# Optimization experiments

Measured on AMD Instinct MI355X. Metric: run time of the kernel, lower is better.

Reference implementation:

```python
import jax, jax.numpy as jnp
import numpy as np

IN_DIM = 512
C_OUT = IN_DIM // 8  # 64
B, H, W = 8, 128, 128


def setup_inputs() -> dict:
    key = jax.random.key(0)
    ks = jax.random.split(key, 6)
    x = jax.random.normal(ks[0], (B, IN_DIM, H, W), dtype=jnp.float32)
    # 1x1 conv weights stored as [out_ch, in_ch] matrices (kernel size 1)
    qkv_w = jax.random.normal(ks[1], (3 * C_OUT, IN_DIM), dtype=jnp.float32) * (1.0 / np.sqrt(IN_DIM))
    qkv_b = jax.random.normal(ks[2], (3 * C_OUT,), dtype=jnp.float32) * 0.01
    out_w = jax.random.normal(ks[3], (IN_DIM, C_OUT), dtype=jnp.float32) * (1.0 / np.sqrt(C_OUT))
    out_b = jax.random.normal(ks[4], (IN_DIM,), dtype=jnp.float32) * 0.01
    # gamma is init to 0 in torch; use a small nonzero value so both paths are exercised
    gamma = jnp.asarray(0.5, dtype=jnp.float32)
    return {"x": x, "qkv_w": qkv_w, "qkv_b": qkv_b, "out_w": out_w, "out_b": out_b, "gamma": gamma}


def reference(x, qkv_w, qkv_b, out_w, out_b, gamma):
    # qkv_conv: 1x1 conv == channel matmul
    qkv = jnp.einsum('bchw,oc->bohw', x, qkv_w) + qkv_b[None, :, None, None]
    q, k, v = jnp.split(qkv, 3, axis=1)  # each [B, C', H, W]

    # Horizontal branch: per column w, channel-channel attention contracting over H
    energy_h = jnp.einsum('bqhw,bkhw->bwqk', q, k)          # [B, W, C', C']
    attn_h = jax.nn.softmax(energy_h, axis=-1)
    out_h = jnp.einsum('bwqk,bkhw->bqhw', attn_h, v)        # [B, C', H, W]

    # Vertical branch: per row h, channel-channel attention contracting over W
    energy_v = jnp.einsum('bqhw,bkhw->bhqk', q, k)          # [B, H, C', C']
    attn_v = jax.nn.softmax(energy_v, axis=-1)
    out_v = jnp.einsum('bhqk,bkhw->bqhw', attn_v, v)        # [B, C', H, W]

    out = gamma * (out_h + out_v)
    out = jnp.einsum('bchw,oc->bohw', out, out_w) + out_b[None, :, None, None]
    return out + x
```

## Files before the change

kernel.cpp:

```cpp
#include <hip/hip_runtime.h>


typedef _Float16 f16;
typedef _Float16 f16x8 __attribute__((ext_vector_type(8)));
typedef float f32x4 __attribute__((ext_vector_type(4)));

#define MFMA16(a, b, c) __builtin_amdgcn_mfma_f32_16x16x32_f16(a, b, c, 0, 0, 0)

constexpr int CIN = 512;
constexpr int COUT = 64;
constexpr int HW = 128;
constexpr int P = HW * HW;
constexpr int QKV_CH = 192;

__global__ __launch_bounds__(256) void qkv_gemm(
    const float* __restrict__ x, const float* __restrict__ w,
    const float* __restrict__ bias, f16* __restrict__ qkv)
{
  __shared__ __attribute__((aligned(16))) f16 Wl[64 * 40];
  __shared__ __attribute__((aligned(16))) f16 Xt[128 * 40];
  const int m0 = blockIdx.x * 64;
  const int p0 = blockIdx.y * 128;
  const int b = blockIdx.z;
  const float* xb = x + (size_t)b * CIN * P;
  const int t = threadIdx.x;
  const int lane = t & 63, wv = t >> 6;
  const int quad = lane >> 4, l15 = lane & 15;
  const int wm = (wv >> 1) * 32, wn = (wv & 1) * 64;

  f32x4 acc[2][4] = {};
  for (int k0 = 0; k0 < CIN; k0 += 32) {
    for (int it = 0; it < 2; ++it) {
      int c = t + it * 256;
      int row = c >> 3, c4 = (c & 7) * 4;
      const float4 v = *(const float4*)(w + (size_t)(m0 + row) * CIN + k0 + c4);
      f16* d = &Wl[row * 40 + c4];
      d[0] = (f16)v.x; d[1] = (f16)v.y; d[2] = (f16)v.z; d[3] = (f16)v.w;
    }
    for (int it = 0; it < 4; ++it) {
      int c = t + it * 256;
      int kr = c >> 5, p4 = (c & 31) * 4;
      const float4 v = *(const float4*)(xb + (size_t)(k0 + kr) * P + p0 + p4);
      float vv[4] = {v.x, v.y, v.z, v.w};
#pragma unroll
      for (int j = 0; j < 4; ++j) {
        int p = p4 + j;
        int kc = kr ^ (((p >> 3) & 3) << 3);
        Xt[p * 40 + kc] = (f16)vv[j];
      }
    }
    __syncthreads();
    f16x8 af[2], bf[4];
#pragma unroll
    for (int ms = 0; ms < 2; ++ms)
      af[ms] = *(const f16x8*)&Wl[(wm + ms * 16 + l15) * 40 + quad * 8];
#pragma unroll
    for (int ns = 0; ns < 4; ++ns) {
      int pr = wn + ns * 16 + l15;
      int kb = (quad * 8) ^ (((pr >> 3) & 3) << 3);
      bf[ns] = *(const f16x8*)&Xt[pr * 40 + kb];
    }
#pragma unroll
    for (int ms = 0; ms < 2; ++ms)
#pragma unroll
      for (int ns = 0; ns < 4; ++ns)
        acc[ms][ns] = MFMA16(af[ms], bf[ns], acc[ms][ns]);
    __syncthreads();
  }
  f16* ob = qkv + (size_t)b * QKV_CH * P;
#pragma unroll
  for (int ms = 0; ms < 2; ++ms) {
    int mbase = m0 + wm + ms * 16 + quad * 4;
#pragma unroll
    for (int r = 0; r < 4; ++r) {
      float bi = bias[mbase + r];
#pragma unroll
      for (int ns = 0; ns < 4; ++ns) {
        int p = p0 + wn + ns * 16 + l15;
        ob[(size_t)(mbase + r) * P + p] = (f16)(acc[ms][ns][r] + bi);
      }
    }
  }
}

__global__ __launch_bounds__(256) void transpose_hw(
    const f16* __restrict__ in, f16* __restrict__ out)
{
  __shared__ __attribute__((aligned(16))) f16 T[64 * 72];
  const size_t plane = blockIdx.x;
  const int r0 = blockIdx.y * 64, c0 = blockIdx.z * 64;
  const f16* ip = in + plane * P;
  f16* op = out + plane * P;
  const int t = threadIdx.x;
  for (int it = 0; it < 2; ++it) {
    int c = t + it * 256;
    int row = c >> 3, c8 = (c & 7) * 8;
    *(f16x8*)&T[row * 72 + c8] =
        *(const f16x8*)(ip + (size_t)(r0 + row) * HW + c0 + c8);
  }
  __syncthreads();
  for (int it = 0; it < 2; ++it) {
    int c = t + it * 256;
    int wr = c >> 3, h8 = (c & 7) * 8;
    f16 tmp[8];
#pragma unroll
    for (int j = 0; j < 8; ++j) tmp[j] = T[(h8 + j) * 72 + wr];
    *(f16x8*)(op + (size_t)(c0 + wr) * HW + r0 + h8) = *(const f16x8*)tmp;
  }
}

__global__ __launch_bounds__(256) void cc_attn(
    const f16* __restrict__ qkvT, const f16* __restrict__ qkvN,
    f16* __restrict__ outT, f16* __restrict__ outN)
{
  __shared__ __attribute__((aligned(16))) f16 smem[64 * 136 * 2 + 128 * 72];
  f16* Ql = smem;
  f16* Kl = smem + 64 * 136;
  f16* Vt = smem + 2 * 64 * 136;
  f16* Al = smem;
  const int s = blockIdx.x, b = blockIdx.y;
  const f16* src = blockIdx.z ? qkvN : qkvT;
  f16* dst = blockIdx.z ? outN : outT;
  const f16* base = src + (size_t)b * QKV_CH * P + (size_t)s * HW;
  const int t = threadIdx.x;
  const int lane = t & 63, wv = t >> 6;
  const int quad = lane >> 4, l15 = lane & 15;

  for (int it = 0; it < 4; ++it) {
    int c = t + it * 256;
    int row = c >> 4, c8 = (c & 15) * 8;
    *(f16x8*)&Ql[row * 136 + c8] = *(const f16x8*)(base + (size_t)row * P + c8);
    *(f16x8*)&Kl[row * 136 + c8] =
        *(const f16x8*)(base + (size_t)(64 + row) * P + c8);
    f16x8 v = *(const f16x8*)(base + (size_t)(128 + row) * P + c8);
#pragma unroll
    for (int j = 0; j < 8; ++j) {
      int h = c8 + j;
      int kc = row ^ (((h >> 3) & 7) << 3);
      Vt[h * 72 + kc] = v[j];
    }
  }
  __syncthreads();

  const int m0 = wv * 16;
  f32x4 e[4] = {};
#pragma unroll
  for (int kk = 0; kk < 4; ++kk) {
    f16x8 aq = *(const f16x8*)&Ql[(m0 + l15) * 136 + kk * 32 + quad * 8];
#pragma unroll
    for (int nt = 0; nt < 4; ++nt) {
      f16x8 bk = *(const f16x8*)&Kl[(nt * 16 + l15) * 136 + kk * 32 + quad * 8];
      e[nt] = MFMA16(aq, bk, e[nt]);
    }
  }
  float pr[4][4];
  float rinv[4];
#pragma unroll
  for (int r = 0; r < 4; ++r) {
    float mx = fmaxf(fmaxf(e[0][r], e[1][r]), fmaxf(e[2][r], e[3][r]));
    for (int off = 1; off < 16; off <<= 1) mx = fmaxf(mx, __shfl_xor(mx, off));
    float sm = 0.f;
#pragma unroll
    for (int nt = 0; nt < 4; ++nt) {
      float pv = __expf(e[nt][r] - mx);
      pr[nt][r] = pv;
      sm += pv;
    }
    for (int off = 1; off < 16; off <<= 1) sm += __shfl_xor(sm, off);
    rinv[r] = 1.0f / sm;
  }
  __syncthreads();
#pragma unroll
  for (int nt = 0; nt < 4; ++nt)
#pragma unroll
    for (int r = 0; r < 4; ++r)
      Al[(m0 + quad * 4 + r) * 72 + nt * 16 + l15] = (f16)(pr[nt][r] * rinv[r]);
  __syncthreads();

  f32x4 o[8] = {};
#pragma unroll
  for (int kk = 0; kk < 2; ++kk) {
    f16x8 ap = *(const f16x8*)&Al[(m0 + l15) * 72 + kk * 32 + quad * 8];
#pragma unroll
    for (int nt = 0; nt < 8; ++nt) {
      int hr = nt * 16 + l15;
      int kb = (kk * 32 + quad * 8) ^ (((hr >> 3) & 7) << 3);
      f16x8 bv = *(const f16x8*)&Vt[hr * 72 + kb];
      o[nt] = MFMA16(ap, bv, o[nt]);
    }
  }
  f16* db = dst + (size_t)b * COUT * P + (size_t)s * HW;
#pragma unroll
  for (int nt = 0; nt < 8; ++nt)
#pragma unroll
    for (int r = 0; r < 4; ++r)
      db[(size_t)(m0 + quad * 4 + r) * P + nt * 16 + l15] = (f16)o[nt][r];
}

__global__ __launch_bounds__(256) void out_proj(
    const f16* __restrict__ ah, const f16* __restrict__ av,
    const float* __restrict__ w, const float* __restrict__ bias,
    const float* __restrict__ gamma_p, const float* __restrict__ x,
    float* __restrict__ out)
{
  __shared__ __attribute__((aligned(16))) f16 Wl[64 * 72];
  __shared__ __attribute__((aligned(16))) f16 St[128 * 72];
  const int m0 = blockIdx.x * 64;
  const int p0 = blockIdx.y * 128;
  const int b = blockIdx.z;
  const int t = threadIdx.x;
  const int lane = t & 63, wv = t >> 6;
  const int quad = lane >> 4, l15 = lane & 15;
  const int wm = (wv >> 1) * 32, wn = (wv & 1) * 64;

  for (int it = 0; it < 4; ++it) {
    int c = t + it * 256;
    int row = c >> 4, c4 = (c & 15) * 4;
    const float4 v = *(const float4*)(w + (size_t)(m0 + row) * COUT + c4);
    f16* d = &Wl[row * 72 + c4];
    d[0] = (f16)v.x; d[1] = (f16)v.y; d[2] = (f16)v.z; d[3] = (f16)v.w;
  }
  const size_t abase = (size_t)b * COUT * P + p0;
  for (int it = 0; it < 4; ++it) {
    int c = t + it * 256;
    int k = c >> 4, p8 = (c & 15) * 8;
    f16x8 a = *(const f16x8*)(ah + abase + (size_t)k * P + p8);
    f16x8 vv = *(const f16x8*)(av + abase + (size_t)k * P + p8);
#pragma unroll
    for (int j = 0; j < 8; ++j) {
      int p = p8 + j;
      int kc = k ^ (((p >> 3) & 7) << 3);
      St[p * 72 + kc] = (f16)(a[j] + vv[j]);
    }
  }
  __syncthreads();

  f32x4 acc[2][4] = {};
#pragma unroll
  for (int kk = 0; kk < 2; ++kk) {
    f16x8 af[2], bf[4];
#pragma unroll
    for (int ms = 0; ms < 2; ++ms)
      af[ms] = *(const f16x8*)&Wl[(wm + ms * 16 + l15) * 72 + kk * 32 + quad * 8];
#pragma unroll
    for (int ns = 0; ns < 4; ++ns) {
      int pr2 = wn + ns * 16 + l15;
      int kb = (kk * 32 + quad * 8) ^ (((pr2 >> 3) & 7) << 3);
      bf[ns] = *(const f16x8*)&St[pr2 * 72 + kb];
    }
#pragma unroll
    for (int ms = 0; ms < 2; ++ms)
#pragma unroll
      for (int ns = 0; ns < 4; ++ns)
        acc[ms][ns] = MFMA16(af[ms], bf[ns], acc[ms][ns]);
  }
  const float g = *gamma_p;
  const float* xb = x + (size_t)b * CIN * P;
  float* ob = out + (size_t)b * CIN * P;
#pragma unroll
  for (int ms = 0; ms < 2; ++ms) {
    int mbase = m0 + wm + ms * 16 + quad * 4;
#pragma unroll
    for (int r = 0; r < 4; ++r) {
      int m = mbase + r;
      float bi = bias[m];
#pragma unroll
      for (int ns = 0; ns < 4; ++ns) {
        int p = p0 + wn + ns * 16 + l15;
        size_t idx = (size_t)m * P + p;
        ob[idx] = g * acc[ms][ns][r] + bi + xb[idx];
      }
    }
  }
}

extern "C" void kernel_launch(void* const* d_in, const int* in_sizes, int n_in,
                              void* d_out, int out_size, void* d_ws,
                              size_t ws_size, hipStream_t stream)
{
  (void)in_sizes; (void)n_in; (void)out_size; (void)ws_size;
  const float* x = (const float*)d_in[0];
  const float* qkv_w = (const float*)d_in[1];
  const float* qkv_b = (const float*)d_in[2];
  const float* out_w = (const float*)d_in[3];
  const float* out_b = (const float*)d_in[4];
  const float* gamma = (const float*)d_in[5];
  float* out = (float*)d_out;

  char* ws = (char*)d_ws;
  const size_t QKV_BYTES = (size_t)8 * QKV_CH * P * sizeof(f16);
  const size_t ATT_BYTES = (size_t)8 * COUT * P * sizeof(f16);
  f16* qkv  = (f16*)ws;
  f16* qkvT = (f16*)(ws + QKV_BYTES);
  f16* ahT  = (f16*)(ws + 2 * QKV_BYTES);
  f16* ahN  = (f16*)(ws + 2 * QKV_BYTES + ATT_BYTES);
  f16* avN  = (f16*)(ws + 2 * QKV_BYTES + 2 * ATT_BYTES);

  qkv_gemm<<<dim3(3, 128, 8), 256, 0, stream>>>(x, qkv_w, qkv_b, qkv);
  transpose_hw<<<dim3(8 * QKV_CH, 2, 2), 256, 0, stream>>>(qkv, qkvT);
  cc_attn<<<dim3(128, 8, 2), 256, 0, stream>>>(qkvT, qkv, ahT, avN);
  transpose_hw<<<dim3(8 * COUT, 2, 2), 256, 0, stream>>>(ahT, ahN);
  out_proj<<<dim3(8, 128, 8), 256, 0, stream>>>(ahN, avN, out_w, out_b, gamma,
                                                x, out);
}
```

Before: 670.5 us.

## Compute all QKV channels per block and swap MFMA operands for vector stores

The QKV projection now has each block compute all 192 output channels for its 128-pixel tile, so the fp32 input tile is read and converted once instead of three times across channel blocks. In both GEMMs the MFMA operands are swapped so each lane's accumulator holds four consecutive pixels. This allows packed f16x4 stores in the QKV GEMM and float4 residual loads and stores in the output projection. In exchange, the QKV kernel uses three times as many accumulator registers and launches a third as many blocks, which may lower occupancy.

```diff
diff --git a/kernel.cpp b/kernel.cpp
--- a/kernel.cpp
+++ b/kernel.cpp
@@ -2,6 +2,7 @@
 
 
 typedef _Float16 f16;
+typedef _Float16 f16x4 __attribute__((ext_vector_type(4)));
 typedef _Float16 f16x8 __attribute__((ext_vector_type(8)));
 typedef float f32x4 __attribute__((ext_vector_type(4)));
 
@@ -17,23 +18,22 @@
     const float* __restrict__ x, const float* __restrict__ w,
     const float* __restrict__ bias, f16* __restrict__ qkv)
 {
-  __shared__ __attribute__((aligned(16))) f16 Wl[64 * 40];
+  __shared__ __attribute__((aligned(16))) f16 Wl[QKV_CH * 40];
   __shared__ __attribute__((aligned(16))) f16 Xt[128 * 40];
-  const int m0 = blockIdx.x * 64;
-  const int p0 = blockIdx.y * 128;
-  const int b = blockIdx.z;
+  const int p0 = blockIdx.x * 128;
+  const int b = blockIdx.y;
   const float* xb = x + (size_t)b * CIN * P;
   const int t = threadIdx.x;
   const int lane = t & 63, wv = t >> 6;
   const int quad = lane >> 4, l15 = lane & 15;
   const int wm = (wv >> 1) * 32, wn = (wv & 1) * 64;
 
-  f32x4 acc[2][4] = {};
+  f32x4 acc[3][4][2] = {};
   for (int k0 = 0; k0 < CIN; k0 += 32) {
-    for (int it = 0; it < 2; ++it) {
+    for (int it = 0; it < 6; ++it) {
       int c = t + it * 256;
       int row = c >> 3, c4 = (c & 7) * 4;
-      const float4 v = *(const float4*)(w + (size_t)(m0 + row) * CIN + k0 + c4);
+      const float4 v = *(const float4*)(w + (size_t)row * CIN + k0 + c4);
       f16* d = &Wl[row * 40 + c4];
       d[0] = (f16)v.x; d[1] = (f16)v.y; d[2] = (f16)v.z; d[3] = (f16)v.w;
     }
@@ -50,34 +50,41 @@
       }
     }
     __syncthreads();
-    f16x8 af[2], bf[4];
-#pragma unroll
-    for (int ms = 0; ms < 2; ++ms)
-      af[ms] = *(const f16x8*)&Wl[(wm + ms * 16 + l15) * 40 + quad * 8];
-#pragma unroll
-    for (int ns = 0; ns < 4; ++ns) {
-      int pr = wn + ns * 16 + l15;
+    f16x8 xf[4];
+#pragma unroll
+    for (int ps = 0; ps < 4; ++ps) {
+      int pr = wn + ps * 16 + l15;
       int kb = (quad * 8) ^ (((pr >> 3) & 3) << 3);
-      bf[ns] = *(const f16x8*)&Xt[pr * 40 + kb];
-    }
-#pragma unroll
-    for (int ms = 0; ms < 2; ++ms)
-#pragma unroll
-      for (int ns = 0; ns < 4; ++ns)
-        acc[ms][ns] = MFMA16(af[ms], bf[ns], acc[ms][ns]);
+      xf[ps] = *(const f16x8*)&Xt[pr * 40 + kb];
+    }
+#pragma unroll
+    for (int mt = 0; mt < 3; ++mt) {
+      f16x8 wf[2];
+#pragma unroll
+      for (int ms = 0; ms < 2; ++ms)
+        wf[ms] = *(const f16x8*)&Wl[(mt * 64 + wm + ms * 16 + l15) * 40 + quad * 8];
+#pragma unroll
+      for (int ps = 0; ps < 4; ++ps)
+#pragma unroll
+        for (int ms = 0; ms < 2; ++ms)
+          acc[mt][ps][ms] = MFMA16(xf[ps], wf[ms], acc[mt][ps][ms]);
+    }
     __syncthreads();
   }
   f16* ob = qkv + (size_t)b * QKV_CH * P;
 #pragma unroll
-  for (int ms = 0; ms < 2; ++ms) {
-    int mbase = m0 + wm + ms * 16 + quad * 4;
-#pragma unroll
-    for (int r = 0; r < 4; ++r) {
-      float bi = bias[mbase + r];
-#pragma unroll
-      for (int ns = 0; ns < 4; ++ns) {
-        int p = p0 + wn + ns * 16 + l15;
-        ob[(size_t)(mbase + r) * P + p] = (f16)(acc[ms][ns][r] + bi);
+  for (int mt = 0; mt < 3; ++mt) {
+#pragma unroll
+    for (int ms = 0; ms < 2; ++ms) {
+      int m = mt * 64 + wm + ms * 16 + l15;
+      float bi = bias[m];
+#pragma unroll
+      for (int ps = 0; ps < 4; ++ps) {
+        int p = p0 + wn + ps * 16 + quad * 4;
+        f16x4 tmp;
+#pragma unroll
+        for (int r = 0; r < 4; ++r) tmp[r] = (f16)(acc[mt][ps][ms][r] + bi);
+        *(f16x4*)(ob + (size_t)m * P + p) = tmp;
       }
     }
   }
@@ -235,41 +242,43 @@
   }
   __syncthreads();
 
-  f32x4 acc[2][4] = {};
+  f32x4 acc[4][2] = {};
 #pragma unroll
   for (int kk = 0; kk < 2; ++kk) {
-    f16x8 af[2], bf[4];
+    f16x8 sf[4], wf[2];
+#pragma unroll
+    for (int ps = 0; ps < 4; ++ps) {
+      int pr2 = wn + ps * 16 + l15;
+      int kb = (kk * 32 + quad * 8) ^ (((pr2 >> 3) & 7) << 3);
+      sf[ps] = *(const f16x8*)&St[pr2 * 72 + kb];
+    }
 #pragma unroll
     for (int ms = 0; ms < 2; ++ms)
-      af[ms] = *(const f16x8*)&Wl[(wm + ms * 16 + l15) * 72 + kk * 32 + quad * 8];
-#pragma unroll
-    for (int ns = 0; ns < 4; ++ns) {
-      int pr2 = wn + ns * 16 + l15;
-      int kb = (kk * 32 + quad * 8) ^ (((pr2 >> 3) & 7) << 3);
-      bf[ns] = *(const f16x8*)&St[pr2 * 72 + kb];
-    }
-#pragma unroll
-    for (int ms = 0; ms < 2; ++ms)
-#pragma unroll
-      for (int ns = 0; ns < 4; ++ns)
-        acc[ms][ns] = MFMA16(af[ms], bf[ns], acc[ms][ns]);
+      wf[ms] = *(const f16x8*)&Wl[(wm + ms * 16 + l15) * 72 + kk * 32 + quad * 8];
+#pragma unroll
+    for (int ps = 0; ps < 4; ++ps)
+#pragma unroll
+      for (int ms = 0; ms < 2; ++ms)
+        acc[ps][ms] = MFMA16(sf[ps], wf[ms], acc[ps][ms]);
   }
   const float g = *gamma_p;
   const float* xb = x + (size_t)b * CIN * P;
   float* ob = out + (size_t)b * CIN * P;
 #pragma unroll
   for (int ms = 0; ms < 2; ++ms) {
-    int mbase = m0 + wm + ms * 16 + quad * 4;
-#pragma unroll
-    for (int r = 0; r < 4; ++r) {
-      int m = mbase + r;
-      float bi = bias[m];
-#pragma unroll
-      for (int ns = 0; ns < 4; ++ns) {
-        int p = p0 + wn + ns * 16 + l15;
-        size_t idx = (size_t)m * P + p;
-        ob[idx] = g * acc[ms][ns][r] + bi + xb[idx];
-      }
+    int m = m0 + wm + ms * 16 + l15;
+    float bi = bias[m];
+#pragma unroll
+    for (int ps = 0; ps < 4; ++ps) {
+      int p = p0 + wn + ps * 16 + quad * 4;
+      size_t idx = (size_t)m * P + p;
+      const float4 xv = *(const float4*)(xb + idx);
+      float4 ov;
+      ov.x = g * acc[ps][ms][0] + bi + xv.x;
+      ov.y = g * acc[ps][ms][1] + bi + xv.y;
+      ov.z = g * acc[ps][ms][2] + bi + xv.z;
+      ov.w = g * acc[ps][ms][3] + bi + xv.w;
+      *(float4*)(ob + idx) = ov;
     }
   }
 }
@@ -296,7 +305,7 @@
   f16* ahN  = (f16*)(ws + 2 * QKV_BYTES + ATT_BYTES);
   f16* avN  = (f16*)(ws + 2 * QKV_BYTES + 2 * ATT_BYTES);
 
-  qkv_gemm<<<dim3(3, 128, 8), 256, 0, stream>>>(x, qkv_w, qkv_b, qkv);
+  qkv_gemm<<<dim3(128, 8), 256, 0, stream>>>(x, qkv_w, qkv_b, qkv);
   transpose_hw<<<dim3(8 * QKV_CH, 2, 2), 256, 0, stream>>>(qkv, qkvT);
   cc_attn<<<dim3(128, 8, 2), 256, 0, stream>>>(qkvT, qkv, ahT, avN);
   transpose_hw<<<dim3(8 * COUT, 2, 2), 256, 0, stream>>>(ahT, ahN);
```

Result: faster. 606.4 us (-9.6%).
